# Performance work log

Hardware: AMD Instinct MI355X
Metric: run time of the kernel (lower is better)

Reference implementation:

```python
import jax, jax.numpy as jnp
import numpy as np


def _three_nn_interp(xyz1, xyz2, feat2):
    # squared Euclidean distances via gram trick, avoids (B,N,S,3) tensor
    # d2: (B, N, S)
    n1 = jnp.sum(xyz1 * xyz1, axis=-1)               # (B, N)
    n2 = jnp.sum(xyz2 * xyz2, axis=-1)               # (B, S)
    d2 = n1[:, :, None] + n2[:, None, :] - 2.0 * jnp.einsum('bnc,bsc->bns', xyz1, xyz2)
    d = jnp.sqrt(jnp.maximum(d2, 0.0))
    k = min(3, xyz2.shape[1])
    neg_d, idx = jax.lax.top_k(-d, k)                # smallest k distances
    dist = jnp.maximum(-neg_d, 1e-10)               # (B, N, k)
    w = 1.0 / dist
    w = w / jnp.sum(w, axis=-1, keepdims=True)
    # gather feat2 at idx: (B, N, k, C2)
    f2 = jnp.take_along_axis(feat2[:, None, :, :], idx[..., None], axis=2)
    return jnp.sum(f2 * w[..., None], axis=2)        # (B, N, C2)


def setup_inputs() -> dict:
    key = jax.random.key(0)
    ks = jax.random.split(key, 8)
    B, N, S, C1, C2, OUT = 8, 8192, 2048, 128, 256, 256
    IN = C1 + C2
    return {
        'xyz1': jax.random.normal(ks[0], (B, N, 3), dtype=jnp.float32),
        'xyz2': jax.random.normal(ks[1], (B, S, 3), dtype=jnp.float32),
        'feat1': jax.random.normal(ks[2], (B, N, C1), dtype=jnp.float32),
        'feat2': jax.random.normal(ks[3], (B, S, C2), dtype=jnp.float32),
        'W1': jax.random.normal(ks[4], (IN, OUT), dtype=jnp.float32) * (1.0 / np.sqrt(IN)),
        'b1': jnp.zeros((OUT,), dtype=jnp.float32),
        'W2': jax.random.normal(ks[5], (OUT, OUT), dtype=jnp.float32) * (1.0 / np.sqrt(OUT)),
        'b2': jnp.zeros((OUT,), dtype=jnp.float32),
    }


def reference(xyz1, xyz2, feat1, feat2, W1, b1, W2, b2):
    if xyz2.shape[1] == 1:
        interp = jnp.broadcast_to(feat2, (feat2.shape[0], xyz1.shape[1], feat2.shape[2]))
    else:
        interp = _three_nn_interp(xyz1, xyz2, feat2)
    x = jnp.concatenate([feat1, interp], axis=-1)    # (B, N, C1+C2)
    x = jax.nn.relu(x @ W1 + b1)
    x = jax.nn.relu(x @ W2 + b2)
    return x
```

## Files before the change

kernel.cpp:

```cpp
#include <hip/hip_runtime.h>
#include <hip/hip_bf16.h>

#define BB   8
#define NN   8192
#define SS   2048
#define C1C  128
#define C2C  256
#define KIN  384
#define OUTC 256

typedef __attribute__((ext_vector_type(4))) float f32x4;
typedef __attribute__((ext_vector_type(8))) short short8;
typedef __attribute__((ext_vector_type(8))) unsigned short ushortx8;

__device__ __forceinline__ ushort f2bf(float v) {
    __hip_bfloat16 h = __float2bfloat16(v);
    return __builtin_bit_cast(ushort, h);
}

__device__ __forceinline__ float med3(float a, float b, float c) {
    return __builtin_amdgcn_fmed3f(a, b, c);
}

__global__ __launch_bounds__(1024, 8) void knn_gather_kernel(
    const float* __restrict__ xyz1, const float* __restrict__ xyz2,
    const float* __restrict__ feat2, ushort* __restrict__ interpB)
{
    __shared__ float4 sp[SS];
    __shared__ int   sIdx[128][3];
    __shared__ float sW[128][3];

    const int tid   = threadIdx.x;
    const int b     = blockIdx.x & 7;
    const int chunk = blockIdx.x >> 3;
    const int qbase = chunk << 7;

    const float* x2 = xyz2 + (size_t)b * SS * 3;
    for (int i = tid; i < SS; i += 1024) {
        float x = x2[i*3+0], y = x2[i*3+1], z = x2[i*3+2];
        sp[i] = make_float4(-2.f*x, -2.f*y, -2.f*z, x*x + y*y + z*z);
    }
    __syncthreads();

    const int g = tid >> 4;
    const int l = tid & 15;
    const int qa = qbase + g * 2;

    const float* qp = xyz1 + ((size_t)b * NN + qa) * 3;
    float px[2] = {qp[0], qp[3]};
    float py[2] = {qp[1], qp[4]};
    float pz[2] = {qp[2], qp[5]};

    float c0[2], c1[2], c2[2];
#pragma unroll
    for (int qi = 0; qi < 2; ++qi) { c0[qi] = c1[qi] = c2[qi] = 1e30f; }

    for (int jj = 0; jj < 128; jj += 4) {
        float4 P[4];
#pragma unroll
        for (int u = 0; u < 4; ++u) P[u] = sp[((jj + u) << 4) + l];
#pragma unroll
        for (int u = 0; u < 4; ++u) {
#pragma unroll
            for (int qi = 0; qi < 2; ++qi) {
                float f = fmaf(px[qi], P[u].x,
                          fmaf(py[qi], P[u].y,
                          fmaf(pz[qi], P[u].z, P[u].w)));
                c2[qi] = med3(f, c1[qi], c2[qi]);
                c1[qi] = med3(f, c0[qi], c1[qi]);
                c0[qi] = fminf(f, c0[qi]);
            }
        }
    }

#pragma unroll
    for (int m = 1; m <= 8; m <<= 1) {
#pragma unroll
        for (int qi = 0; qi < 2; ++qi) {
            float b0 = __shfl_xor(c0[qi], m);
            float b1 = __shfl_xor(c1[qi], m);
            float b2 = __shfl_xor(c2[qi], m);
            float bv[3] = {b0, b1, b2};
#pragma unroll
            for (int e = 0; e < 3; ++e) {
                float d = bv[e];
                c2[qi] = med3(d, c1[qi], c2[qi]);
                c1[qi] = med3(d, c0[qi], c1[qi]);
                c0[qi] = fminf(d, c0[qi]);
            }
        }
    }
    const float t0 = c2[0], t1 = c2[1];

    float e0[2], e1[2], e2[2];
    int   i0[2], i1[2], i2[2];
#pragma unroll
    for (int qi = 0; qi < 2; ++qi) {
        e0[qi] = e1[qi] = e2[qi] = 1e30f;
        i0[qi] = i1[qi] = i2[qi] = 0x3fffffff;
    }

    for (int jj = 0; jj < 128; jj += 4) {
        float4 P[4];
#pragma unroll
        for (int u = 0; u < 4; ++u) P[u] = sp[((jj + u) << 4) + l];
#pragma unroll
        for (int u = 0; u < 4; ++u) {
            const int s = ((jj + u) << 4) + l;
#pragma unroll
            for (int qi = 0; qi < 2; ++qi) {
                float f = fmaf(px[qi], P[u].x,
                          fmaf(py[qi], P[u].y,
                          fmaf(pz[qi], P[u].z, P[u].w)));
                float tq = qi ? t1 : t0;
                if (f <= tq) {
                    bool lt2 = (f < e2[qi]) || (f == e2[qi] && s < i2[qi]);
                    if (lt2) {
                        bool lt1 = (f < e1[qi]) || (f == e1[qi] && s < i1[qi]);
                        bool lt0 = (f < e0[qi]) || (f == e0[qi] && s < i0[qi]);
                        e2[qi] = lt1 ? e1[qi] : f;  i2[qi] = lt1 ? i1[qi] : s;
                        e1[qi] = lt0 ? e0[qi] : (lt1 ? f : e1[qi]);
                        i1[qi] = lt0 ? i0[qi] : (lt1 ? s : i1[qi]);
                        e0[qi] = lt0 ? f : e0[qi];  i0[qi] = lt0 ? s : i0[qi];
                    }
                }
            }
        }
    }

#pragma unroll
    for (int m = 1; m <= 8; m <<= 1) {
#pragma unroll
        for (int qi = 0; qi < 2; ++qi) {
            float ob0 = __shfl_xor(e0[qi], m), ob1 = __shfl_xor(e1[qi], m), ob2 = __shfl_xor(e2[qi], m);
            int   oj0 = __shfl_xor(i0[qi], m), oj1 = __shfl_xor(i1[qi], m), oj2 = __shfl_xor(i2[qi], m);
            float dv[3] = {ob0, ob1, ob2}; int iv[3] = {oj0, oj1, oj2};
#pragma unroll
            for (int e = 0; e < 3; ++e) {
                float d = dv[e]; int s = iv[e];
                bool lt2 = (d < e2[qi]) || (d == e2[qi] && s < i2[qi]);
                if (lt2) {
                    bool lt1 = (d < e1[qi]) || (d == e1[qi] && s < i1[qi]);
                    bool lt0 = (d < e0[qi]) || (d == e0[qi] && s < i0[qi]);
                    e2[qi] = lt1 ? e1[qi] : d;  i2[qi] = lt1 ? i1[qi] : s;
                    e1[qi] = lt0 ? e0[qi] : (lt1 ? d : e1[qi]);
                    i1[qi] = lt0 ? i0[qi] : (lt1 ? s : i1[qi]);
                    e0[qi] = lt0 ? d : e0[qi];  i0[qi] = lt0 ? s : i0[qi];
                }
            }
        }
    }

    if (l == 0) {
#pragma unroll
        for (int qi = 0; qi < 2; ++qi) {
            float nx = px[qi], ny = py[qi], nz = pz[qi];
            float n1 = nx*nx + ny*ny + nz*nz;
            float d0 = sqrtf(fmaxf(n1 + e0[qi], 0.f));
            float d1 = sqrtf(fmaxf(n1 + e1[qi], 0.f));
            float d2s = sqrtf(fmaxf(n1 + e2[qi], 0.f));
            float w0 = 1.f / fmaxf(d0, 1e-10f);
            float w1 = 1.f / fmaxf(d1, 1e-10f);
            float w2 = 1.f / fmaxf(d2s, 1e-10f);
            float wsum = w0 + w1 + w2;
            int qq = g * 2 + qi;
            sIdx[qq][0] = i0[qi]; sIdx[qq][1] = i1[qi]; sIdx[qq][2] = i2[qi];
            sW[qq][0] = w0 / wsum; sW[qq][1] = w1 / wsum; sW[qq][2] = w2 / wsum;
        }
    }
    __syncthreads();

    const int wid = tid >> 6, lane = tid & 63;
    for (int qq = wid; qq < 128; qq += 16) {
        int a0 = sIdx[qq][0], a1 = sIdx[qq][1], a2 = sIdx[qq][2];
        float w0 = sW[qq][0], w1 = sW[qq][1], w2 = sW[qq][2];
        const float4* r0 = (const float4*)(feat2 + ((size_t)b * SS + a0) * C2C);
        const float4* r1 = (const float4*)(feat2 + ((size_t)b * SS + a1) * C2C);
        const float4* r2 = (const float4*)(feat2 + ((size_t)b * SS + a2) * C2C);
        float4 v0 = r0[lane], v1 = r1[lane], v2 = r2[lane];
        ushort4 o;
        o.x = f2bf(w0*v0.x + w1*v1.x + w2*v2.x);
        o.y = f2bf(w0*v0.y + w1*v1.y + w2*v2.y);
        o.z = f2bf(w0*v0.z + w1*v1.z + w2*v2.z);
        o.w = f2bf(w0*v0.w + w1*v1.w + w2*v2.w);
        *(ushort4*)(interpB + ((size_t)b * NN + qbase + qq) * C2C + lane * 4) = o;
    }
}

__global__ __launch_bounds__(256) void transpose_cvt_both_kernel(
    const float* __restrict__ W1, ushort* __restrict__ W1t,
    const float* __restrict__ W2, ushort* __restrict__ W2t)
{
    int idx = blockIdx.x * 256 + threadIdx.x;
    const int n1 = KIN * OUTC;
    if (idx < n1) {
        int n = idx / KIN, k = idx - n * KIN;
        W1t[idx] = f2bf(W1[(size_t)k * OUTC + n]);
    } else {
        int j = idx - n1;
        if (j < OUTC * OUTC) {
            int n = j / OUTC, k = j - n * OUTC;
            W2t[j] = f2bf(W2[(size_t)k * OUTC + n]);
        }
    }
}

#define GBM 128
#define GBN 256
#define GBK 32

__device__ __forceinline__ void gld_lds16(const void* g, void* l) {
    __builtin_amdgcn_global_load_lds(
        (const __attribute__((address_space(1))) void*)g,
        (__attribute__((address_space(3))) void*)l, 16, 0, 0);
}

__global__ __launch_bounds__(512, 4) void gemm_fused(
    const float* __restrict__ feat1,
    const ushort* __restrict__ interpB,
    const ushort* __restrict__ W1t, const float* __restrict__ b1,
    const ushort* __restrict__ W2t, const float* __restrict__ b2,
    float* __restrict__ out)
{
    __shared__ ushort pool[GBM * 256];
    __shared__ ushort sB2[GBN * GBK];

    const int tid  = threadIdx.x;
    const int lane = tid & 63;
    const int wid  = tid >> 6;
    const int m0   = blockIdx.x * GBM;
    const int wr   = wid >> 2;
    const int wc   = wid & 3;

    const int rsub = lane >> 2;
    const int slot = lane & 3;
    const int csub = slot * 8;
    const int usw  = (slot ^ (rsub & 3)) * 8;

    const int kgrp = (lane >> 4) * 8;
    const int rl   = lane & 15;
    const int ksw  = kgrp ^ ((rl & 3) << 3);
    const int cl   = lane & 15;
    const int rgrp = (lane >> 4) * 4;

    auto stageAB = [&](int k0, int buf) {
        ushort* sAb = pool + buf * 12288;
        ushort* sBb = sAb + 4096;
#pragma unroll
        for (int c = 0; c < 3; ++c) {
            const int cid = wid * 3 + c;
            if (cid < 8) {
                const int r = m0 + cid * 16 + rsub;
                if (k0 < C1C) {
                    const float* src = feat1 + (size_t)r * C1C + k0 + usw;
                    float4 u = ((const float4*)src)[0];
                    float4 v = ((const float4*)src)[1];
                    ushortx8 t;
                    t[0] = f2bf(u.x); t[1] = f2bf(u.y); t[2] = f2bf(u.z); t[3] = f2bf(u.w);
                    t[4] = f2bf(v.x); t[5] = f2bf(v.y); t[6] = f2bf(v.z); t[7] = f2bf(v.w);
                    *(ushortx8*)&sAb[cid * 512 + rsub * 32 + csub] = t;
                } else {
                    gld_lds16(interpB + (size_t)r * C2C + (k0 - C1C) + usw, &sAb[cid * 512]);
                }
            } else {
                const int bi = cid - 8;
                const int r = bi * 16 + rsub;
                gld_lds16(W1t + (size_t)r * KIN + k0 + usw, &sBb[bi * 512]);
            }
        }
    };

    f32x4 acc1[4][4];
#pragma unroll
    for (int i = 0; i < 4; ++i)
#pragma unroll
        for (int j = 0; j < 4; ++j) acc1[i][j] = (f32x4){0.f, 0.f, 0.f, 0.f};

    int cur = 0;
    stageAB(0, 0);
    for (int k0 = 0; k0 < KIN; k0 += GBK) {
        __syncthreads();
        if (k0 + GBK < KIN) stageAB(k0 + GBK, cur ^ 1);

        const ushort* sAb = pool + cur * 12288;
        const ushort* sBb = sAb + 4096;
        short8 af[4], bf[4];
#pragma unroll
        for (int i = 0; i < 4; ++i) {
            af[i] = *(const short8*)&sAb[(wr * 64 + i * 16 + rl) * GBK + ksw];
            bf[i] = *(const short8*)&sBb[(wc * 64 + i * 16 + rl) * GBK + ksw];
        }
#pragma unroll
        for (int i = 0; i < 4; ++i)
#pragma unroll
            for (int j = 0; j < 4; ++j)
                acc1[i][j] = __builtin_amdgcn_mfma_f32_16x16x32_bf16(
                    af[i], bf[j], acc1[i][j], 0, 0, 0);
        cur ^= 1;
    }
    __syncthreads();

#pragma unroll
    for (int c = 0; c < 2; ++c) {
        const int cid = wid * 2 + c;
        const int r = cid * 16 + rsub;
        gld_lds16(W2t + (size_t)r * OUTC + 0 + usw, &sB2[cid * 512]);
    }

#pragma unroll
    for (int j = 0; j < 4; ++j) {
        const int c = wc * 64 + j * 16 + cl;
        const float bv = b1[c];
        const int u = c >> 3, sub = c & 7;
#pragma unroll
        for (int i = 0; i < 4; ++i) {
#pragma unroll
            for (int rr = 0; rr < 4; ++rr) {
                const int r = wr * 64 + i * 16 + rgrp + rr;
                const float v = fmaxf(acc1[i][j][rr] + bv, 0.f);
                pool[r * 256 + ((u ^ (r & 31)) << 3) + sub] = f2bf(v);
            }
        }
    }
    __syncthreads();

    f32x4 acc2[4][4];
#pragma unroll
    for (int i = 0; i < 4; ++i)
#pragma unroll
        for (int j = 0; j < 4; ++j) acc2[i][j] = (f32x4){0.f, 0.f, 0.f, 0.f};

    for (int k0 = 0; k0 < OUTC; k0 += GBK) {
        short8 af[4], bf[4];
        const int ub = (k0 >> 3) + (lane >> 4);
#pragma unroll
        for (int i = 0; i < 4; ++i) {
            const int r = wr * 64 + i * 16 + rl;
            af[i] = *(const short8*)&pool[r * 256 + ((ub ^ (r & 31)) << 3)];
            bf[i] = *(const short8*)&sB2[(wc * 64 + i * 16 + rl) * GBK + ksw];
        }
#pragma unroll
        for (int i = 0; i < 4; ++i)
#pragma unroll
            for (int j = 0; j < 4; ++j)
                acc2[i][j] = __builtin_amdgcn_mfma_f32_16x16x32_bf16(
                    af[i], bf[j], acc2[i][j], 0, 0, 0);

        const int kn = k0 + GBK;
        __syncthreads();
        if (kn < OUTC) {
#pragma unroll
            for (int c = 0; c < 2; ++c) {
                const int cid = wid * 2 + c;
                const int r = cid * 16 + rsub;
                gld_lds16(W2t + (size_t)r * OUTC + kn + usw, &sB2[cid * 512]);
            }
            __syncthreads();
        }
    }

#pragma unroll
    for (int j = 0; j < 4; ++j) {
        const int col = wc * 64 + j * 16 + cl;
        const float bv = b2[col];
#pragma unroll
        for (int i = 0; i < 4; ++i) {
            const int rowb = m0 + wr * 64 + i * 16 + rgrp;
#pragma unroll
            for (int rr = 0; rr < 4; ++rr) {
                out[(size_t)(rowb + rr) * OUTC + col] =
                    fmaxf(acc2[i][j][rr] + bv, 0.f);
            }
        }
    }
}

extern "C" void kernel_launch(void* const* d_in, const int* in_sizes, int n_in,
                              void* d_out, int out_size, void* d_ws, size_t ws_size,
                              hipStream_t stream) {
    const float* xyz1  = (const float*)d_in[0];
    const float* xyz2  = (const float*)d_in[1];
    const float* feat1 = (const float*)d_in[2];
    const float* feat2 = (const float*)d_in[3];
    const float* W1    = (const float*)d_in[4];
    const float* b1    = (const float*)d_in[5];
    const float* W2    = (const float*)d_in[6];
    const float* b2    = (const float*)d_in[7];
    float* out = (float*)d_out;

    char* ws = (char*)d_ws;
    ushort* interpB = (ushort*)(ws);
    ushort* W1t     = (ushort*)(ws + 33554432);
    ushort* W2t     = (ushort*)(ws + 33751040);

    const int M = BB * NN;

    transpose_cvt_both_kernel<<<(KIN * OUTC + OUTC * OUTC + 255) / 256, 256, 0, stream>>>(
        W1, W1t, W2, W2t);

    knn_gather_kernel<<<512, 1024, 0, stream>>>(xyz1, xyz2, feat2, interpB);

    gemm_fused<<<M / GBM, 512, 0, stream>>>(feat1, interpB, W1t, b1, W2t, b2, out);
}
```

Baseline: 110.6 us.

## Fuse three-NN feature interpolation into GEMM A-tile staging

The kNN kernel no longer gathers and interpolates feat2 into a bf16 intermediate. It writes only the neighbor indices and normalized weights per query (32 bytes each). The GEMM's A-tile staging now reads those, gathers the three feat2 rows, blends them, and converts to bf16 directly into LDS. This drops the 32 MB interpolated-feature write and read-back. In exchange the GEMM staging does synchronous scattered gathers in place of async global-to-LDS loads, which may stall its pipeline.

```diff
diff --git a/kernel.cpp b/kernel.cpp
--- a/kernel.cpp
+++ b/kernel.cpp
@@ -22,13 +22,11 @@
     return __builtin_amdgcn_fmed3f(a, b, c);
 }
 
-__global__ __launch_bounds__(1024, 8) void knn_gather_kernel(
+__global__ __launch_bounds__(1024, 8) void knn_kernel(
     const float* __restrict__ xyz1, const float* __restrict__ xyz2,
-    const float* __restrict__ feat2, ushort* __restrict__ interpB)
+    char* __restrict__ nnbuf)
 {
     __shared__ float4 sp[SS];
-    __shared__ int   sIdx[128][3];
-    __shared__ float sW[128][3];
 
     const int tid   = threadIdx.x;
     const int b     = blockIdx.x & 7;
@@ -163,27 +161,14 @@
             float w1 = 1.f / fmaxf(d1, 1e-10f);
             float w2 = 1.f / fmaxf(d2s, 1e-10f);
             float wsum = w0 + w1 + w2;
-            int qq = g * 2 + qi;
-            sIdx[qq][0] = i0[qi]; sIdx[qq][1] = i1[qi]; sIdx[qq][2] = i2[qi];
-            sW[qq][0] = w0 / wsum; sW[qq][1] = w1 / wsum; sW[qq][2] = w2 / wsum;
-        }
-    }
-    __syncthreads();
-
-    const int wid = tid >> 6, lane = tid & 63;
-    for (int qq = wid; qq < 128; qq += 16) {
-        int a0 = sIdx[qq][0], a1 = sIdx[qq][1], a2 = sIdx[qq][2];
-        float w0 = sW[qq][0], w1 = sW[qq][1], w2 = sW[qq][2];
-        const float4* r0 = (const float4*)(feat2 + ((size_t)b * SS + a0) * C2C);
-        const float4* r1 = (const float4*)(feat2 + ((size_t)b * SS + a1) * C2C);
-        const float4* r2 = (const float4*)(feat2 + ((size_t)b * SS + a2) * C2C);
-        float4 v0 = r0[lane], v1 = r1[lane], v2 = r2[lane];
-        ushort4 o;
-        o.x = f2bf(w0*v0.x + w1*v1.x + w2*v2.x);
-        o.y = f2bf(w0*v0.y + w1*v1.y + w2*v2.y);
-        o.z = f2bf(w0*v0.z + w1*v1.z + w2*v2.z);
-        o.w = f2bf(w0*v0.w + w1*v1.w + w2*v2.w);
-        *(ushort4*)(interpB + ((size_t)b * NN + qbase + qq) * C2C + lane * 4) = o;
+            size_t qg = (size_t)b * NN + qa + qi;
+            int*   np = (int*)(nnbuf + qg * 32);
+            float* wp = (float*)(nnbuf + qg * 32 + 16);
+            np[0] = b * SS + i0[qi];
+            np[1] = b * SS + i1[qi];
+            np[2] = b * SS + i2[qi];
+            wp[0] = w0 / wsum; wp[1] = w1 / wsum; wp[2] = w2 / wsum;
+        }
     }
 }
 
@@ -217,7 +202,8 @@
 
 __global__ __launch_bounds__(512, 4) void gemm_fused(
     const float* __restrict__ feat1,
-    const ushort* __restrict__ interpB,
+    const float* __restrict__ feat2,
+    const char* __restrict__ nnbuf,
     const ushort* __restrict__ W1t, const float* __restrict__ b1,
     const ushort* __restrict__ W2t, const float* __restrict__ b2,
     float* __restrict__ out)
@@ -260,7 +246,29 @@
                     t[4] = f2bf(v.x); t[5] = f2bf(v.y); t[6] = f2bf(v.z); t[7] = f2bf(v.w);
                     *(ushortx8*)&sAb[cid * 512 + rsub * 32 + csub] = t;
                 } else {
-                    gld_lds16(interpB + (size_t)r * C2C + (k0 - C1C) + usw, &sAb[cid * 512]);
+                    const char* nr = nnbuf + (size_t)r * 32;
+                    const int4   iv = *(const int4*)nr;
+                    const float4 wv = *(const float4*)(nr + 16);
+                    const int kc = (k0 - C1C) + usw;
+                    const float* p0 = feat2 + (size_t)iv.x * C2C + kc;
+                    const float* p1 = feat2 + (size_t)iv.y * C2C + kc;
+                    const float* p2 = feat2 + (size_t)iv.z * C2C + kc;
+                    float4 a0 = ((const float4*)p0)[0];
+                    float4 a1 = ((const float4*)p1)[0];
+                    float4 a2 = ((const float4*)p2)[0];
+                    ushortx8 t;
+                    t[0] = f2bf(wv.x*a0.x + wv.y*a1.x + wv.z*a2.x);
+                    t[1] = f2bf(wv.x*a0.y + wv.y*a1.y + wv.z*a2.y);
+                    t[2] = f2bf(wv.x*a0.z + wv.y*a1.z + wv.z*a2.z);
+                    t[3] = f2bf(wv.x*a0.w + wv.y*a1.w + wv.z*a2.w);
+                    float4 b0 = ((const float4*)p0)[1];
+                    float4 b1v = ((const float4*)p1)[1];
+                    float4 b2v = ((const float4*)p2)[1];
+                    t[4] = f2bf(wv.x*b0.x + wv.y*b1v.x + wv.z*b2v.x);
+                    t[5] = f2bf(wv.x*b0.y + wv.y*b1v.y + wv.z*b2v.y);
+                    t[6] = f2bf(wv.x*b0.z + wv.y*b1v.z + wv.z*b2v.z);
+                    t[7] = f2bf(wv.x*b0.w + wv.y*b1v.w + wv.z*b2v.w);
+                    *(ushortx8*)&sAb[cid * 512 + rsub * 32 + csub] = t;
                 }
             } else {
                 const int bi = cid - 8;
@@ -389,16 +397,17 @@
     float* out = (float*)d_out;
 
     char* ws = (char*)d_ws;
-    ushort* interpB = (ushort*)(ws);
-    ushort* W1t     = (ushort*)(ws + 33554432);
-    ushort* W2t     = (ushort*)(ws + 33751040);
+    char*   nnbuf = ws;
+    ushort* W1t   = (ushort*)(ws + 2097152);
+    ushort* W2t   = (ushort*)(ws + 2293760);
 
     const int M = BB * NN;
 
     transpose_cvt_both_kernel<<<(KIN * OUTC + OUTC * OUTC + 255) / 256, 256, 0, stream>>>(
         W1, W1t, W2, W2t);
 
-    knn_gather_kernel<<<512, 1024, 0, stream>>>(xyz1, xyz2, feat2, interpB);
-
-    gemm_fused<<<M / GBM, 512, 0, stream>>>(feat1, interpB, W1t, b1, W2t, b2, out);
-}
+    knn_kernel<<<512, 1024, 0, stream>>>(xyz1, xyz2, nnbuf);
+
+    gemm_fused<<<M / GBM, 512, 0, stream>>>(feat1, feat2, nnbuf,
+                                            W1t, b1, W2t, b2, out);
+}
```

New measurement: 121.0 us. 1.09x slower.

## Pre-pack W2 into MFMA fragment layout and load directly to registers

Applied to the files above, without the earlier changes.

The weight prep kernel now writes W2 in a layout that matches the per-lane MFMA B-fragment order, so each wave can read its B operands straight from global memory with one 16-byte load per fragment. The second GEMM stage drops the LDS staging buffer for W2 and the two barriers per k-step, and instead prefetches the next k-step's fragments into registers (double buffering). This removes synchronisation and LDS traffic. In exchange it adds register pressure, and every wave re-reads W2 from global memory or cache instead of sharing one copy in LDS.

```diff
diff --git a/kernel.cpp b/kernel.cpp
--- a/kernel.cpp
+++ b/kernel.cpp
@@ -187,9 +187,9 @@
     }
 }
 
-__global__ __launch_bounds__(256) void transpose_cvt_both_kernel(
+__global__ __launch_bounds__(256) void weights_prep_kernel(
     const float* __restrict__ W1, ushort* __restrict__ W1t,
-    const float* __restrict__ W2, ushort* __restrict__ W2t)
+    const float* __restrict__ W2, ushort* __restrict__ W2pack)
 {
     int idx = blockIdx.x * 256 + threadIdx.x;
     const int n1 = KIN * OUTC;
@@ -197,10 +197,13 @@
         int n = idx / KIN, k = idx - n * KIN;
         W1t[idx] = f2bf(W1[(size_t)k * OUTC + n]);
     } else {
-        int j = idx - n1;
-        if (j < OUTC * OUTC) {
-            int n = j / OUTC, k = j - n * OUTC;
-            W2t[j] = f2bf(W2[(size_t)k * OUTC + n]);
+        int o = idx - n1;
+        if (o < OUTC * OUTC) {
+            int e = o & 7, lane = (o >> 3) & 63, j = (o >> 9) & 3;
+            int wc = (o >> 11) & 3, s = o >> 13;
+            int n = wc * 64 + j * 16 + (lane & 15);
+            int k = s * 32 + (lane >> 4) * 8 + e;
+            W2pack[o] = f2bf(W2[(size_t)k * OUTC + n]);
         }
     }
 }
@@ -219,11 +222,10 @@
     const float* __restrict__ feat1,
     const ushort* __restrict__ interpB,
     const ushort* __restrict__ W1t, const float* __restrict__ b1,
-    const ushort* __restrict__ W2t, const float* __restrict__ b2,
+    const ushort* __restrict__ W2pack, const float* __restrict__ b2,
     float* __restrict__ out)
 {
     __shared__ ushort pool[GBM * 256];
-    __shared__ ushort sB2[GBN * GBK];
 
     const int tid  = threadIdx.x;
     const int lane = tid & 63;
@@ -300,12 +302,10 @@
     }
     __syncthreads();
 
-#pragma unroll
-    for (int c = 0; c < 2; ++c) {
-        const int cid = wid * 2 + c;
-        const int r = cid * 16 + rsub;
-        gld_lds16(W2t + (size_t)r * OUTC + 0 + usw, &sB2[cid * 512]);
-    }
+    short8 bfc[4], bfn[4];
+#pragma unroll
+    for (int j = 0; j < 4; ++j)
+        bfc[j] = *(const short8*)&W2pack[(size_t)(0 * 16 + wc * 4 + j) * 512 + lane * 8];
 
 #pragma unroll
     for (int j = 0; j < 4; ++j) {
@@ -330,33 +330,27 @@
 #pragma unroll
         for (int j = 0; j < 4; ++j) acc2[i][j] = (f32x4){0.f, 0.f, 0.f, 0.f};
 
-    for (int k0 = 0; k0 < OUTC; k0 += GBK) {
-        short8 af[4], bf[4];
-        const int ub = (k0 >> 3) + (lane >> 4);
+    for (int s = 0; s < 8; ++s) {
+        if (s < 7) {
+#pragma unroll
+            for (int j = 0; j < 4; ++j)
+                bfn[j] = *(const short8*)&W2pack[(size_t)((s + 1) * 16 + wc * 4 + j) * 512 + lane * 8];
+        }
+        const int ub = s * 4 + (lane >> 4);
+        short8 af[4];
 #pragma unroll
         for (int i = 0; i < 4; ++i) {
             const int r = wr * 64 + i * 16 + rl;
             af[i] = *(const short8*)&pool[r * 256 + ((ub ^ (r & 31)) << 3)];
-            bf[i] = *(const short8*)&sB2[(wc * 64 + i * 16 + rl) * GBK + ksw];
         }
 #pragma unroll
         for (int i = 0; i < 4; ++i)
 #pragma unroll
             for (int j = 0; j < 4; ++j)
                 acc2[i][j] = __builtin_amdgcn_mfma_f32_16x16x32_bf16(
-                    af[i], bf[j], acc2[i][j], 0, 0, 0);
-
-        const int kn = k0 + GBK;
-        __syncthreads();
-        if (kn < OUTC) {
-#pragma unroll
-            for (int c = 0; c < 2; ++c) {
-                const int cid = wid * 2 + c;
-                const int r = cid * 16 + rsub;
-                gld_lds16(W2t + (size_t)r * OUTC + kn + usw, &sB2[cid * 512]);
-            }
-            __syncthreads();
-        }
+                    af[i], bfc[j], acc2[i][j], 0, 0, 0);
+#pragma unroll
+        for (int j = 0; j < 4; ++j) bfc[j] = bfn[j];
     }
 
 #pragma unroll
@@ -391,14 +385,15 @@
     char* ws = (char*)d_ws;
     ushort* interpB = (ushort*)(ws);
     ushort* W1t     = (ushort*)(ws + 33554432);
-    ushort* W2t     = (ushort*)(ws + 33751040);
+    ushort* W2pack  = (ushort*)(ws + 33751040);
 
     const int M = BB * NN;
 
-    transpose_cvt_both_kernel<<<(KIN * OUTC + OUTC * OUTC + 255) / 256, 256, 0, stream>>>(
-        W1, W1t, W2, W2t);
+    weights_prep_kernel<<<(KIN * OUTC + OUTC * OUTC + 255) / 256, 256, 0, stream>>>(
+        W1, W1t, W2, W2pack);
 
     knn_gather_kernel<<<512, 1024, 0, stream>>>(xyz1, xyz2, feat2, interpB);
 
-    gemm_fused<<<M / GBM, 512, 0, stream>>>(feat1, interpB, W1t, b1, W2t, b2, out);
-}
+    gemm_fused<<<M / GBM, 512, 0, stream>>>(feat1, interpB,
+                                            W1t, b1, W2pack, b2, out);
+}
```

Measured after the change: 104.6 us. -5.4%, faster.
